# Optimization experiments

Hardware: AMD Instinct MI355X
Metric: run time of the kernel (lower is better)

The kernel has to match this reference:

```python
import jax, jax.numpy as jnp
import numpy as np

N = 50000
E = 800000
F_IN = 128
H = 128
OUT = 2


def _init_linear(key, fan_in, fan_out):
    kw, kb = jax.random.split(key)
    bound = 1.0 / np.sqrt(fan_in)
    W = jax.random.uniform(kw, (fan_in, fan_out), jnp.float32, -bound, bound)
    b = jax.random.uniform(kb, (fan_out,), jnp.float32, -bound, bound)
    return W, b


def setup_inputs() -> dict:
    key = jax.random.key(0)
    ks = jax.random.split(key, 8)
    x = jax.random.normal(ks[0], (N, F_IN), jnp.float32)
    edge_index = jax.random.randint(ks[1], (2, E), 0, N, jnp.int64)
    # layer 0: in=F_IN -> out=H ; MLP([2*F_IN, H, H])
    w1_0, b1_0 = _init_linear(ks[2], 2 * F_IN, H)
    w2_0, b2_0 = _init_linear(ks[3], H, H)
    # layer 1: in=H -> out=H ; MLP([2*H, H, H])
    w1_1, b1_1 = _init_linear(ks[4], 2 * H, H)
    w2_1, b2_1 = _init_linear(ks[5], H, H)
    # layer 2 (last): in=H -> out=OUT ; MLP([2*H, OUT, OUT])
    w1_2, b1_2 = _init_linear(ks[6], 2 * H, OUT)
    w2_2, b2_2 = _init_linear(ks[7], OUT, OUT)
    return {"x": x, "edge_index": edge_index,
            "w1_0": w1_0, "b1_0": b1_0, "w2_0": w2_0, "b2_0": b2_0,
            "w1_1": w1_1, "b1_1": b1_1, "w2_1": w2_1, "b2_1": b2_1,
            "w1_2": w1_2, "b1_2": b1_2, "w2_2": w2_2, "b2_2": b2_2}


def _edge_conv(x, src, dst, W1, b1, W2, b2):
    # message on edge (j->i): MLP(concat[x_i, x_j - x_i]); max-aggregate at i
    xi = x[dst]                       # [E, F]
    xj = x[src]                       # [E, F]
    feat = jnp.concatenate([xi, xj - xi], axis=-1)   # [E, 2F]
    msg = jnp.maximum(feat @ W1 + b1, 0.0) @ W2 + b2  # [E, out]
    agg = jax.ops.segment_max(msg, dst, num_segments=N)
    # nodes with no incoming edges get 0 (PyG scatter-max convention)
    return jnp.where(jnp.isneginf(agg), 0.0, agg)


def reference(x, edge_index, w1_0, b1_0, w2_0, b2_0,
              w1_1, b1_1, w2_1, b2_1, w1_2, b1_2, w2_2, b2_2):
    src = edge_index[0]
    dst = edge_index[1]
    h = _edge_conv(x, src, dst, w1_0, b1_0, w2_0, b2_0)
    h = jnp.maximum(h, 0.0)  # inter-layer ReLU (dropout skipped: eval mode)
    h = _edge_conv(h, src, dst, w1_1, b1_1, w2_1, b2_1)
    h = jnp.maximum(h, 0.0)
    out = _edge_conv(h, src, dst, w1_2, b1_2, w2_2, b2_2)  # [N, 2]
    return out
```

## Files before the change

### kernel.cpp

```cpp
#include <hip/hip_runtime.h>
#include <cstdint>
#include <cstddef>


#define KEY_NEGINF 0x007FFFFFu

typedef __attribute__((ext_vector_type(8))) short bf16x8;
typedef __attribute__((ext_vector_type(4))) float f32x4;

__device__ __forceinline__ unsigned fkey(float f) {
  unsigned u = __float_as_uint(f);
  return (u & 0x80000000u) ? ~u : (u | 0x80000000u);
}
__device__ __forceinline__ float funkey(unsigned k) {
  unsigned u = (k & 0x80000000u) ? (k & 0x7FFFFFFFu) : ~k;
  return __uint_as_float(u);
}
__device__ __forceinline__ unsigned short f2bf(float f) {
  unsigned u = __float_as_uint(f);
  unsigned r = u + 0x7FFFu + ((u >> 16) & 1u);
  return (unsigned short)(r >> 16);
}
__device__ __forceinline__ float bflo(unsigned u) { return __uint_as_float(u << 16); }
__device__ __forceinline__ float bfhi(unsigned u) { return __uint_as_float(u & 0xFFFF0000u); }
__device__ __forceinline__ unsigned pack2(unsigned a, unsigned b) {
  float lo = fmaxf(bflo(a) + bflo(b), 0.f);
  float hi = fmaxf(bfhi(a) + bfhi(b), 0.f);
  return (unsigned)f2bf(lo) | ((unsigned)f2bf(hi) << 16);
}

__global__ void build_wcatbf(const float* __restrict__ w1, unsigned short* __restrict__ wcg) {
  int i = blockIdx.x * 256 + threadIdx.x;
  if (i >= 256 * 16) return;
  int n = i >> 4, c = i & 15;
  alignas(16) unsigned short ob[8];
  #pragma unroll
  for (int j = 0; j < 8; ++j) {
    int k = c * 8 + j;
    float v;
    if (n < 128) v = w1[(size_t)k * 128 + n] - w1[(size_t)(128 + k) * 128 + n];
    else         v = w1[(size_t)(128 + k) * 128 + (n - 128)];
    ob[j] = f2bf(v);
  }
  *reinterpret_cast<uint4*>(&wcg[n * 128 + ((c ^ (n & 7)) * 8)]) =
      *reinterpret_cast<const uint4*>(ob);
}

__global__ void build_w2bf(const float* __restrict__ w2, unsigned short* __restrict__ wlg) {
  int i = blockIdx.x * 256 + threadIdx.x;
  if (i >= 128 * 16) return;
  int n = i >> 4, c = i & 15;
  alignas(16) unsigned short ob[8];
  #pragma unroll
  for (int j = 0; j < 8; ++j) ob[j] = f2bf(w2[(size_t)(c * 8 + j) * 128 + n]);
  *reinterpret_cast<uint4*>(&wlg[n * 128 + ((c ^ (n & 7)) * 8)]) =
      *reinterpret_cast<const uint4*>(ob);
}

__global__ void build_wcat(const float* __restrict__ w1, float* __restrict__ wcat,
                           int F, int O) {
  int i = blockIdx.x * 256 + threadIdx.x;
  int total = F * O;
  if (i >= total) return;
  int k = i / O, o = i - k * O;
  float wa = w1[(size_t)k * O + o];
  float wb = w1[(size_t)(F + k) * O + o];
  wcat[(size_t)k * 2 * O + o] = wa - wb;
  wcat[(size_t)k * 2 * O + O + o] = wb;
}

__global__ void fill_u32(unsigned* __restrict__ p, unsigned v, size_t n) {
  size_t i = (size_t)blockIdx.x * blockDim.x + threadIdx.x;
  size_t stride = (size_t)gridDim.x * blockDim.x;
  for (; i < n; i += stride) p[i] = v;
}

__global__ void final_out(const unsigned* __restrict__ p, float* __restrict__ out, size_t n) {
  size_t i = (size_t)blockIdx.x * blockDim.x + threadIdx.x;
  size_t stride = (size_t)gridDim.x * blockDim.x;
  for (; i < n; i += stride) {
    unsigned k = p[i];
    out[i] = (k == KEY_NEGINF) ? 0.0f : funkey(k);
  }
}

__global__ __launch_bounds__(256, 2) void node_mfma(
    const unsigned* __restrict__ hin, int decode,
    const unsigned short* __restrict__ wcg, const float* __restrict__ b1,
    unsigned short* __restrict__ Abf, unsigned short* __restrict__ Bbf, int nN) {
  __shared__ unsigned short at[64 * 128];
  __shared__ unsigned short wt[256 * 128];
  int t = threadIdx.x;
  {
    const uint4* src = reinterpret_cast<const uint4*>(wcg);
    uint4* dst = reinterpret_cast<uint4*>(wt);
    for (int i = t; i < 4096; i += 256) dst[i] = src[i];
  }
  int m_base = blockIdx.x * 64;
  {
    int r = t >> 2, q = t & 3;
    int gm = min(m_base + r, nN - 1);
    const uint4* src = reinterpret_cast<const uint4*>(hin + (size_t)gm * 128);
    #pragma unroll
    for (int j = 0; j < 4; ++j) {
      int c = q + 4 * j;
      uint4 u0 = src[c * 2], u1 = src[c * 2 + 1];
      unsigned b[8] = {u0.x, u0.y, u0.z, u0.w, u1.x, u1.y, u1.z, u1.w};
      alignas(16) unsigned short ob[8];
      #pragma unroll
      for (int e = 0; e < 8; ++e) {
        float v = decode ? fmaxf(funkey(b[e]), 0.f) : __uint_as_float(b[e]);
        ob[e] = f2bf(v);
      }
      *reinterpret_cast<uint4*>(&at[r * 128 + ((c ^ (r & 7)) * 8)]) =
          *reinterpret_cast<const uint4*>(ob);
    }
  }
  __syncthreads();

  int l = t & 63, w = t >> 6;
  int strip = w * 16, lr = l & 15, lh = l >> 4;
  int arow = strip + lr, erow = strip + lh * 4;

  bf16x8 af[4];
  #pragma unroll
  for (int ks = 0; ks < 4; ++ks)
    af[ks] = *reinterpret_cast<const bf16x8*>(
        &at[arow * 128 + (((ks * 4 + lh) ^ (arow & 7)) * 8)]);

  #pragma unroll
  for (int nt = 0; nt < 16; ++nt) {
    f32x4 acc = (f32x4){0.f, 0.f, 0.f, 0.f};
    int n = nt * 16 + lr;
    #pragma unroll
    for (int ks = 0; ks < 4; ++ks) {
      bf16x8 bf = *reinterpret_cast<const bf16x8*>(
          &wt[n * 128 + (((ks * 4 + lh) ^ (n & 7)) * 8)]);
      acc = __builtin_amdgcn_mfma_f32_16x16x32_bf16(af[ks], bf, acc, 0, 0, 0);
    }
    bool isA = (n < 128);
    float bias = isA ? b1[n] : 0.f;
    int coln = isA ? n : n - 128;
    unsigned short* plane = isA ? Abf : Bbf;
    #pragma unroll
    for (int j = 0; j < 4; ++j) {
      int gm = m_base + erow + j;
      if (gm < nN) plane[(size_t)gm * 128 + coln] = f2bf(acc[j] + bias);
    }
  }
}

__global__ __launch_bounds__(256, 3) void edge_mfma(
    const unsigned short* __restrict__ Abf, const unsigned short* __restrict__ Bbf,
    const int* __restrict__ ei, const unsigned short* __restrict__ wlg,
    const float* __restrict__ b2, unsigned* __restrict__ aggk, int E_) {
  __shared__ unsigned short hs[64 * 128];
  __shared__ unsigned short wl[128 * 128];
  __shared__ int dstl[64];
  int t = threadIdx.x;
  {
    const uint4* src = reinterpret_cast<const uint4*>(wlg);
    uint4* dst = reinterpret_cast<uint4*>(wl);
    for (int i = t; i < 2048; i += 256) dst[i] = src[i];
  }
  int l = t & 63, w = t >> 6;
  int strip = w * 16, lr = l & 15, lh = l >> 4;
  int arow = strip + lr, erow = strip + lh * 4;
  int r = t >> 2, q = t & 3;

  float bb[8];
  #pragma unroll
  for (int nt = 0; nt < 8; ++nt) bb[nt] = b2[nt * 16 + lr];

  int ntiles = (E_ + 63) >> 6;
  int tile = blockIdx.x;
  uint4 ga[4], gb[4];
  int nd = 0;
  if (tile < ntiles) {
    int e = min(tile * 64 + r, E_ - 1);
    int s = ei[e], d = ei[E_ + e];
    const uint4* Ar = reinterpret_cast<const uint4*>(Abf + (size_t)d * 128);
    const uint4* Br = reinterpret_cast<const uint4*>(Bbf + (size_t)s * 128);
    #pragma unroll
    for (int j = 0; j < 4; ++j) { ga[j] = Ar[q + 4 * j]; gb[j] = Br[q + 4 * j]; }
    nd = ei[E_ + min(tile * 64 + t, E_ - 1)];
  }

  for (; tile < ntiles; tile += gridDim.x) {
    __syncthreads();
    #pragma unroll
    for (int j = 0; j < 4; ++j) {
      int c = q + 4 * j;
      uint4 o;
      o.x = pack2(ga[j].x, gb[j].x);
      o.y = pack2(ga[j].y, gb[j].y);
      o.z = pack2(ga[j].z, gb[j].z);
      o.w = pack2(ga[j].w, gb[j].w);
      *reinterpret_cast<uint4*>(&hs[r * 128 + ((c ^ (r & 7)) * 8)]) = o;
    }
    if (t < 64) dstl[t] = nd;
    __syncthreads();

    int next = tile + gridDim.x;
    if (next < ntiles) {
      int e = min(next * 64 + r, E_ - 1);
      int s = ei[e], d = ei[E_ + e];
      const uint4* Ar = reinterpret_cast<const uint4*>(Abf + (size_t)d * 128);
      const uint4* Br = reinterpret_cast<const uint4*>(Bbf + (size_t)s * 128);
      #pragma unroll
      for (int j = 0; j < 4; ++j) { ga[j] = Ar[q + 4 * j]; gb[j] = Br[q + 4 * j]; }
      nd = ei[E_ + min(next * 64 + t, E_ - 1)];
    }

    int drow[4];
    #pragma unroll
    for (int j = 0; j < 4; ++j) drow[j] = dstl[erow + j];
    unsigned cur[8][4];
    #pragma unroll
    for (int nt = 0; nt < 8; ++nt) {
      int col = nt * 16 + lr;
      #pragma unroll
      for (int j = 0; j < 4; ++j)
        cur[nt][j] = aggk[(size_t)drow[j] * 128 + col];
    }

    bf16x8 af[4];
    #pragma unroll
    for (int ks = 0; ks < 4; ++ks)
      af[ks] = *reinterpret_cast<const bf16x8*>(
          &hs[arow * 128 + (((ks * 4 + lh) ^ (arow & 7)) * 8)]);

    #pragma unroll
    for (int nt = 0; nt < 8; ++nt) {
      f32x4 acc = (f32x4){0.f, 0.f, 0.f, 0.f};
      int n = nt * 16 + lr;
      #pragma unroll
      for (int ks = 0; ks < 4; ++ks) {
        bf16x8 bf = *reinterpret_cast<const bf16x8*>(
            &wl[n * 128 + (((ks * 4 + lh) ^ (n & 7)) * 8)]);
        acc = __builtin_amdgcn_mfma_f32_16x16x32_bf16(af[ks], bf, acc, 0, 0, 0);
      }
      #pragma unroll
      for (int j = 0; j < 4; ++j) {
        unsigned key = fkey(acc[j] + bb[nt]);
        if (key > cur[nt][j])
          atomicMax(aggk + (size_t)drow[j] * 128 + n, key);
      }
    }
  }
}

__global__ void node_thin(const unsigned* __restrict__ hin, const float* __restrict__ wcat2,
                          const float* __restrict__ b1, float* __restrict__ AB2,
                          int nNodes) {
  __shared__ float w[128 * 4];
  int t = threadIdx.x;
  if (t < 128) *reinterpret_cast<float4*>(&w[t * 4]) =
      reinterpret_cast<const float4*>(wcat2)[t];
  __syncthreads();
  int node = blockIdx.x * 64 + (t >> 2);
  int o = t & 3;
  if (node >= nNodes) return;
  const uint4* h4 = reinterpret_cast<const uint4*>(hin + (size_t)node * 128);
  float acc = 0.f;
  #pragma unroll 8
  for (int kk = 0; kk < 32; ++kk) {
    uint4 x = h4[kk];
    acc += fmaxf(funkey(x.x), 0.f) * w[(kk * 4 + 0) * 4 + o];
    acc += fmaxf(funkey(x.y), 0.f) * w[(kk * 4 + 1) * 4 + o];
    acc += fmaxf(funkey(x.z), 0.f) * w[(kk * 4 + 2) * 4 + o];
    acc += fmaxf(funkey(x.w), 0.f) * w[(kk * 4 + 3) * 4 + o];
  }
  if (o < 2) acc += b1[o];
  AB2[(size_t)node * 4 + o] = acc;
}

__global__ void edge_small(const float* __restrict__ AB2, const int* __restrict__ ei,
                           const float* __restrict__ w2, const float* __restrict__ b2,
                           unsigned* __restrict__ aggk2, int E_) {
  int e = blockIdx.x * 256 + threadIdx.x;
  if (e >= E_) return;
  int s = ei[e];
  int d = ei[E_ + e];
  float2 a = *reinterpret_cast<const float2*>(AB2 + (size_t)d * 4);
  float2 b = *reinterpret_cast<const float2*>(AB2 + (size_t)s * 4 + 2);
  float h0 = fmaxf(a.x + b.x, 0.f);
  float h1 = fmaxf(a.y + b.y, 0.f);
  float m0 = h0 * w2[0] + h1 * w2[2] + b2[0];
  float m1 = h0 * w2[1] + h1 * w2[3] + b2[1];
  atomicMax(aggk2 + (size_t)d * 2 + 0, fkey(m0));
  atomicMax(aggk2 + (size_t)d * 2 + 1, fkey(m1));
}

extern "C" void kernel_launch(void* const* d_in, const int* in_sizes, int n_in,
                              void* d_out, int out_size, void* d_ws, size_t ws_size,
                              hipStream_t stream) {
  const float* x    = (const float*)d_in[0];
  const int*   ei   = (const int*)d_in[1];
  const float* w1_0 = (const float*)d_in[2];
  const float* b1_0 = (const float*)d_in[3];
  const float* w2_0 = (const float*)d_in[4];
  const float* b2_0 = (const float*)d_in[5];
  const float* w1_1 = (const float*)d_in[6];
  const float* b1_1 = (const float*)d_in[7];
  const float* w2_1 = (const float*)d_in[8];
  const float* b2_1 = (const float*)d_in[9];
  const float* w1_2 = (const float*)d_in[10];
  const float* b1_2 = (const float*)d_in[11];
  const float* w2_2 = (const float*)d_in[12];
  const float* b2_2 = (const float*)d_in[13];

  const int N = in_sizes[0] / 128;
  const int E = in_sizes[1] / 2;

  char* ws = (char*)d_ws;
  const size_t NB = (size_t)N * 128 * 4;
  const size_t HB = (size_t)N * 128 * 2;
  unsigned*       Z    = (unsigned*)(ws);
  unsigned short* Abf  = (unsigned short*)(ws + NB);
  unsigned short* Bbf  = (unsigned short*)(ws + NB + HB);
  float*    AB2  = (float*)(ws + NB + 2 * HB);
  unsigned* agg2 = (unsigned*)(ws + NB + 2 * HB + (size_t)N * 16);
  char*     wp   = ws + NB + 2 * HB + (size_t)N * 16 + (size_t)N * 8;
  unsigned short* wcg0 = (unsigned short*)(wp);
  unsigned short* wcg1 = (unsigned short*)(wp + 65536);
  unsigned short* wlg0 = (unsigned short*)(wp + 131072);
  unsigned short* wlg1 = (unsigned short*)(wp + 163840);
  float*          wc2  = (float*)(wp + 196608);

  const int nb = (N + 63) / 64;
  const int eb = (E + 63) / 64;
  const int egrid = eb < 768 ? eb : 768;
  const size_t nH = (size_t)N * 128;

  build_wcatbf<<<16, 256, 0, stream>>>(w1_0, wcg0);
  build_wcatbf<<<16, 256, 0, stream>>>(w1_1, wcg1);
  build_w2bf<<<8, 256, 0, stream>>>(w2_0, wlg0);
  build_w2bf<<<8, 256, 0, stream>>>(w2_1, wlg1);
  build_wcat<<<1, 256, 0, stream>>>(w1_2, wc2, 128, 2);

  node_mfma<<<nb, 256, 0, stream>>>((const unsigned*)x, 0, wcg0, b1_0, Abf, Bbf, N);
  fill_u32<<<1024, 256, 0, stream>>>(Z, KEY_NEGINF, nH);
  edge_mfma<<<egrid, 256, 0, stream>>>(Abf, Bbf, ei, wlg0, b2_0, Z, E);

  node_mfma<<<nb, 256, 0, stream>>>(Z, 1, wcg1, b1_1, Abf, Bbf, N);
  fill_u32<<<1024, 256, 0, stream>>>(Z, KEY_NEGINF, nH);
  edge_mfma<<<egrid, 256, 0, stream>>>(Abf, Bbf, ei, wlg1, b2_1, Z, E);

  node_thin<<<nb, 256, 0, stream>>>(Z, wc2, b1_2, AB2, N);
  fill_u32<<<256, 256, 0, stream>>>(agg2, KEY_NEGINF, (size_t)N * 2);
  edge_small<<<(E + 255) / 256, 256, 0, stream>>>(AB2, ei, w2_2, b2_2, agg2, E);
  final_out<<<((size_t)N * 2 + 255) / 256, 256, 0, stream>>>(agg2, (float*)d_out, (size_t)N * 2);
}
```

Measured before the change: 734.2 us.

## Sort edges by destination and merge same-destination maxes before atomics

Adds a counting sort of edges by destination node (histogram, single-block scan, atomic scatter) at the start of each call, and feeds the sorted src/dst arrays to all edge kernels. In edge_mfma, consecutive rows sharing a destination are max-reduced in registers before issuing atomicMax, which cuts the number of atomics and improves locality of the aggregation and A-row gathers. The cost is extra preprocessing kernels, including a serial one-block scan over 50k bins, plus extra workspace. The scatter order within a bin is nondeterministic, but max-aggregation makes the result order-independent.

```diff
diff --git a/kernel.cpp b/kernel.cpp
--- a/kernel.cpp
+++ b/kernel.cpp
@@ -27,6 +27,48 @@
   float lo = fmaxf(bflo(a) + bflo(b), 0.f);
   float hi = fmaxf(bfhi(a) + bfhi(b), 0.f);
   return (unsigned)f2bf(lo) | ((unsigned)f2bf(hi) << 16);
+}
+
+__global__ void hist_dst(const int* __restrict__ ei, unsigned* __restrict__ hist, int E_) {
+  int e = blockIdx.x * 256 + threadIdx.x;
+  if (e < E_) atomicAdd(&hist[ei[E_ + e]], 1u);
+}
+
+__global__ void scan_bins(const unsigned* __restrict__ hist, unsigned* __restrict__ offs, int n) {
+  __shared__ unsigned tmp[2][256];
+  __shared__ unsigned carry;
+  int t = threadIdx.x;
+  if (t == 0) carry = 0;
+  __syncthreads();
+  for (int base = 0; base < n; base += 256) {
+    unsigned v = (base + t < n) ? hist[base + t] : 0;
+    int cur = 0;
+    tmp[0][t] = v;
+    __syncthreads();
+    #pragma unroll
+    for (int off = 1; off < 256; off <<= 1) {
+      unsigned add = (t >= off) ? tmp[cur][t - off] : 0;
+      __syncthreads();
+      tmp[cur ^ 1][t] = tmp[cur][t] + add;
+      __syncthreads();
+      cur ^= 1;
+    }
+    unsigned incl = tmp[cur][t];
+    if (base + t < n) offs[base + t] = carry + incl - v;
+    __syncthreads();
+    if (t == 255) carry += incl;
+    __syncthreads();
+  }
+}
+
+__global__ void scatter_edges(const int* __restrict__ ei, unsigned* __restrict__ offs,
+                              int* __restrict__ esrc, int* __restrict__ edst, int E_) {
+  int e = blockIdx.x * 256 + threadIdx.x;
+  if (e >= E_) return;
+  int s = ei[e], d = ei[E_ + e];
+  unsigned pos = atomicAdd(&offs[d], 1u);
+  esrc[pos] = s;
+  edst[pos] = d;
 }
 
 __global__ void build_wcatbf(const float* __restrict__ w1, unsigned short* __restrict__ wcg) {
@@ -152,7 +194,8 @@
 
 __global__ __launch_bounds__(256, 3) void edge_mfma(
     const unsigned short* __restrict__ Abf, const unsigned short* __restrict__ Bbf,
-    const int* __restrict__ ei, const unsigned short* __restrict__ wlg,
+    const int* __restrict__ esrc, const int* __restrict__ edst,
+    const unsigned short* __restrict__ wlg,
     const float* __restrict__ b2, unsigned* __restrict__ aggk, int E_) {
   __shared__ unsigned short hs[64 * 128];
   __shared__ unsigned short wl[128 * 128];
@@ -178,12 +221,12 @@
   int nd = 0;
   if (tile < ntiles) {
     int e = min(tile * 64 + r, E_ - 1);
-    int s = ei[e], d = ei[E_ + e];
+    int s = esrc[e], d = edst[e];
     const uint4* Ar = reinterpret_cast<const uint4*>(Abf + (size_t)d * 128);
     const uint4* Br = reinterpret_cast<const uint4*>(Bbf + (size_t)s * 128);
     #pragma unroll
     for (int j = 0; j < 4; ++j) { ga[j] = Ar[q + 4 * j]; gb[j] = Br[q + 4 * j]; }
-    nd = ei[E_ + min(tile * 64 + t, E_ - 1)];
+    nd = edst[min(tile * 64 + t, E_ - 1)];
   }
 
   for (; tile < ntiles; tile += gridDim.x) {
@@ -204,12 +247,12 @@
     int next = tile + gridDim.x;
     if (next < ntiles) {
       int e = min(next * 64 + r, E_ - 1);
-      int s = ei[e], d = ei[E_ + e];
+      int s = esrc[e], d = edst[e];
       const uint4* Ar = reinterpret_cast<const uint4*>(Abf + (size_t)d * 128);
       const uint4* Br = reinterpret_cast<const uint4*>(Bbf + (size_t)s * 128);
       #pragma unroll
       for (int j = 0; j < 4; ++j) { ga[j] = Ar[q + 4 * j]; gb[j] = Br[q + 4 * j]; }
-      nd = ei[E_ + min(next * 64 + t, E_ - 1)];
+      nd = edst[min(next * 64 + t, E_ - 1)];
     }
 
     int drow[4];
@@ -240,12 +283,20 @@
             &wl[n * 128 + (((ks * 4 + lh) ^ (n & 7)) * 8)]);
         acc = __builtin_amdgcn_mfma_f32_16x16x32_bf16(af[ks], bf, acc, 0, 0, 0);
       }
+      unsigned kcur = fkey(acc[0] + bb[nt]);
       #pragma unroll
-      for (int j = 0; j < 4; ++j) {
-        unsigned key = fkey(acc[j] + bb[nt]);
-        if (key > cur[nt][j])
-          atomicMax(aggk + (size_t)drow[j] * 128 + n, key);
+      for (int j = 1; j < 4; ++j) {
+        unsigned kn = fkey(acc[j] + bb[nt]);
+        if (drow[j] == drow[j - 1]) {
+          kcur = kcur > kn ? kcur : kn;
+        } else {
+          if (kcur > cur[nt][j - 1])
+            atomicMax(aggk + (size_t)drow[j - 1] * 128 + n, kcur);
+          kcur = kn;
+        }
       }
+      if (kcur > cur[nt][3])
+        atomicMax(aggk + (size_t)drow[3] * 128 + n, kcur);
     }
   }
 }
@@ -275,13 +326,14 @@
   AB2[(size_t)node * 4 + o] = acc;
 }
 
-__global__ void edge_small(const float* __restrict__ AB2, const int* __restrict__ ei,
+__global__ void edge_small(const float* __restrict__ AB2, const int* __restrict__ esrc,
+                           const int* __restrict__ edst,
                            const float* __restrict__ w2, const float* __restrict__ b2,
                            unsigned* __restrict__ aggk2, int E_) {
   int e = blockIdx.x * 256 + threadIdx.x;
   if (e >= E_) return;
-  int s = ei[e];
-  int d = ei[E_ + e];
+  int s = esrc[e];
+  int d = edst[e];
   float2 a = *reinterpret_cast<const float2*>(AB2 + (size_t)d * 4);
   float2 b = *reinterpret_cast<const float2*>(AB2 + (size_t)s * 4 + 2);
   float h0 = fmaxf(a.x + b.x, 0.f);
@@ -327,11 +379,22 @@
   unsigned short* wlg0 = (unsigned short*)(wp + 131072);
   unsigned short* wlg1 = (unsigned short*)(wp + 163840);
   float*          wc2  = (float*)(wp + 196608);
+  char*     sp   = wp + 198656;
+  unsigned* hist = (unsigned*)(sp);
+  unsigned* offs = (unsigned*)(sp + (size_t)N * 4);
+  int*      esrc = (int*)(sp + (size_t)N * 8);
+  int*      edst = (int*)(sp + (size_t)N * 8 + (size_t)E * 4);
 
   const int nb = (N + 63) / 64;
   const int eb = (E + 63) / 64;
   const int egrid = eb < 768 ? eb : 768;
+  const int epb = (E + 255) / 256;
   const size_t nH = (size_t)N * 128;
+
+  fill_u32<<<256, 256, 0, stream>>>(hist, 0u, (size_t)N);
+  hist_dst<<<epb, 256, 0, stream>>>(ei, hist, E);
+  scan_bins<<<1, 256, 0, stream>>>(hist, offs, N);
+  scatter_edges<<<epb, 256, 0, stream>>>(ei, offs, esrc, edst, E);
 
   build_wcatbf<<<16, 256, 0, stream>>>(w1_0, wcg0);
   build_wcatbf<<<16, 256, 0, stream>>>(w1_1, wcg1);
@@ -341,14 +404,14 @@
 
   node_mfma<<<nb, 256, 0, stream>>>((const unsigned*)x, 0, wcg0, b1_0, Abf, Bbf, N);
   fill_u32<<<1024, 256, 0, stream>>>(Z, KEY_NEGINF, nH);
-  edge_mfma<<<egrid, 256, 0, stream>>>(Abf, Bbf, ei, wlg0, b2_0, Z, E);
+  edge_mfma<<<egrid, 256, 0, stream>>>(Abf, Bbf, esrc, edst, wlg0, b2_0, Z, E);
 
   node_mfma<<<nb, 256, 0, stream>>>(Z, 1, wcg1, b1_1, Abf, Bbf, N);
   fill_u32<<<1024, 256, 0, stream>>>(Z, KEY_NEGINF, nH);
-  edge_mfma<<<egrid, 256, 0, stream>>>(Abf, Bbf, ei, wlg1, b2_1, Z, E);
+  edge_mfma<<<egrid, 256, 0, stream>>>(Abf, Bbf, esrc, edst, wlg1, b2_1, Z, E);
 
   node_thin<<<nb, 256, 0, stream>>>(Z, wc2, b1_2, AB2, N);
   fill_u32<<<256, 256, 0, stream>>>(agg2, KEY_NEGINF, (size_t)N * 2);
-  edge_small<<<(E + 255) / 256, 256, 0, stream>>>(AB2, ei, w2_2, b2_2, agg2, E);
+  edge_small<<<epb, 256, 0, stream>>>(AB2, esrc, edst, w2_2, b2_2, agg2, E);
   final_out<<<((size_t)N * 2 + 255) / 256, 256, 0, stream>>>(agg2, (float*)d_out, (size_t)N * 2);
 }
```

Result: slower. 988.3 us (+34.6%).
